# Performance work log

Hardware: AMD Instinct MI355X
Metric: run time of the kernel (lower is better)

The kernel has to match this reference:

```python
import jax, jax.numpy as jnp
import numpy as np

B_SZ, T, N, H = 8, 4096, 256, 512  # batch, seq, num_neurons, d_hidden
RMAX, RMIN = 0.99, 0.4


def _glorot_half(k, shape):
    # VarianceScaling(scale=0.5, mode='fan_avg', distribution='uniform')
    fan_avg = (shape[0] + shape[1]) / 2.0
    limit = float(np.sqrt(3.0 * 0.5 / fan_avg))
    return jax.random.uniform(k, shape, jnp.float32, -limit, limit)


def setup_inputs() -> dict:
    key = jax.random.key(0)
    ks = jax.random.split(key, 8)
    x = jax.random.normal(ks[0], (B_SZ, T, N), jnp.float32)
    C_re = _glorot_half(ks[1], (H, N))
    C_im = _glorot_half(ks[2], (H, N))
    B_re = _glorot_half(ks[3], (N, H))
    B_im = _glorot_half(ks[4], (N, H))
    D = jax.random.normal(ks[5], (N,), jnp.float32)
    numin = float(np.log(-np.log(RMAX)))
    numax = float(np.log(-np.log(RMIN)))
    nu = jax.random.uniform(ks[6], (H,), jnp.float32, numin, numax)
    theta = jax.random.uniform(ks[7], (H,), jnp.float32, 0.0, 3.14 / 10)
    lam_abs = jnp.exp(-jnp.exp(nu))  # |lambda| = |exp(-exp(nu) + i*theta)|
    gamma_log = jnp.log(jnp.sqrt(1.0 - lam_abs ** 2))
    return dict(x=x, B_re=B_re, B_im=B_im, C_re=C_re, C_im=C_im,
                D=D, nu=nu, theta=theta, gamma_log=gamma_log)


def _binary_op(qi, qj):
    A_i, b_i = qi
    A_j, b_j = qj
    return (A_j * A_i, A_j * b_i + b_j)


def reference(x, B_re, B_im, C_re, C_im, D, nu, theta, gamma_log):
    u = x  # adapter is identity since n_in == num_neurons
    lam_log = jax.lax.complex(-jnp.exp(nu), theta)            # (H,) log-lambda
    lam = jnp.exp(lam_log)                                     # (H,) diagonal transition
    gamma = jnp.exp(gamma_log).astype(jnp.complex64)           # (H,)
    Bm = jax.lax.complex(B_re, B_im)                           # (N,H)
    Cm = jax.lax.complex(C_re, C_im)                           # (H,N)
    u_c = u.astype(jnp.complex64)
    bu = gamma * (u_c @ Bm)                                    # (B,T,H) complex64
    A = jnp.broadcast_to(lam, (1, u.shape[1], lam.shape[0]))   # (1,T,H), broadcasts in op
    _, xs = jax.lax.associative_scan(_binary_op, (A, bu), axis=1)  # (B,T,H)
    y = jnp.real(xs @ Cm) + D * u                              # (B,T,N) float32
    return y
```

## Files before the change

kernel.cpp:

```cpp
#include <hip/hip_runtime.h>

#define B_SZ 8
#define T_LEN 4096
#define N_DIM 256
#define H_DIM 512
#define NC 32
#define CL 128
#define ROWS (B_SZ * T_LEN)

#define BM 128
#define BN 128
#define BKg 32

typedef __attribute__((ext_vector_type(4))) float f32x4;
typedef __attribute__((ext_vector_type(8))) short bf16x8;

static __device__ __forceinline__ unsigned short f2bf(float f) {
    unsigned int u = __float_as_uint(f);
    unsigned int r = (u + 0x7FFFu + ((u >> 16) & 1u)) >> 16;
    return (unsigned short)r;
}
static __device__ __forceinline__ float bf2f(unsigned short s) {
    return __uint_as_float(((unsigned int)s) << 16);
}

static __device__ __forceinline__ void lam_of(const float* __restrict__ nu,
                                              const float* __restrict__ theta,
                                              int h, float& lre, float& lim) {
    float r = __expf(-__expf(nu[h]));
    float th = theta[h];
    lre = r * __cosf(th);
    lim = r * __sinf(th);
}

__global__ __launch_bounds__(256) void conv_x(const float4* __restrict__ x, ushort4* __restrict__ xb) {
    int id = blockIdx.x * 256 + threadIdx.x;
    float4 v = x[id];
    ushort4 o;
    o.x = f2bf(v.x); o.y = f2bf(v.y); o.z = f2bf(v.z); o.w = f2bf(v.w);
    xb[id] = o;
}

__global__ __launch_bounds__(256) void conv_Bt(const float* __restrict__ Bre,
                                               const float* __restrict__ Bim,
                                               unsigned short* __restrict__ BT1) {
    int id = blockIdx.x * 256 + threadIdx.x;
    int k = id >> 9, h = id & 511;
    BT1[(long)(2 * h) * 256 + k]     = f2bf(Bre[id]);
    BT1[(long)(2 * h + 1) * 256 + k] = f2bf(Bim[id]);
}

__global__ __launch_bounds__(256) void conv_Ct(const float* __restrict__ Cre,
                                               const float* __restrict__ Cim,
                                               unsigned short* __restrict__ CT) {
    int id = blockIdx.x * 256 + threadIdx.x;
    int h = id >> 8, nn = id & 255;
    CT[(long)nn * 1024 + 2 * h]     = f2bf(Cre[id]);
    CT[(long)nn * 1024 + 2 * h + 1] = f2bf(-Cim[id]);
}

template <int MODE>
__global__ __launch_bounds__(256) void gemm_mfma(const unsigned short* __restrict__ A,
                                                 const unsigned short* __restrict__ Bt,
                                                 int M, int N, int K,
                                                 const float* __restrict__ e0,
                                                 const float* __restrict__ e1,
                                                 const unsigned short* __restrict__ e1b,
                                                 void* __restrict__ out) {
    __shared__ unsigned short As[3][BM * BKg];
    __shared__ unsigned short Bs[3][BN * BKg];
    const int tid = threadIdx.x;
    const int lane = tid & 63;
    const int wave = tid >> 6;
    const int wr = wave >> 1, wc = wave & 1;

    const int nwg = (int)gridDim.x;
    const int cpx = nwg >> 3;
    const int bid = (int)blockIdx.x;
    const int tile = (bid & 7) * cpx + (bid >> 3);

    const int nTilesN = N / BN;
    const long tileM = (long)(tile / nTilesN) * BM;
    const long tileN = (long)(tile % nTilesN) * BN;

    const int rsub = lane >> 2;
    const int sg = 8 * ((lane & 3) ^ ((lane >> 3) & 3));
    const unsigned short* Abase = A + tileM * (long)K + sg;
    const unsigned short* Bbase = Bt + tileN * (long)K + sg;

    auto stage = [&](int buf, int k0) {
#pragma unroll
        for (int cc = 0; cc < 2; ++cc) {
            const int c = wave + cc * 4;
            const int row = c * 16 + rsub;
            const unsigned short* ga = Abase + (long)row * K + k0;
            __builtin_amdgcn_global_load_lds((const __attribute__((address_space(1))) unsigned int*)ga,
                                             (__attribute__((address_space(3))) unsigned int*)(As[buf] + c * 512),
                                             16, 0, 0);
            const unsigned short* gb = Bbase + (long)row * K + k0;
            __builtin_amdgcn_global_load_lds((const __attribute__((address_space(1))) unsigned int*)gb,
                                             (__attribute__((address_space(3))) unsigned int*)(Bs[buf] + c * 512),
                                             16, 0, 0);
        }
    };

    const int rdA = 16 * ((lane >> 4) ^ ((lane >> 1) & 3));

    f32x4 acc[4][4] = {};
    const int nt = K / BKg;

    stage(0, 0);
    stage(1, BKg);

    int cur = 0, pf = 2;
    for (int t = 0; t < nt; ++t) {
        if (t + 2 < nt) {
            stage(pf, (t + 2) * BKg);
            asm volatile("s_waitcnt vmcnt(8)" ::: "memory");
        } else if (t + 1 < nt) {
            asm volatile("s_waitcnt vmcnt(4)" ::: "memory");
        } else {
            asm volatile("s_waitcnt vmcnt(0)" ::: "memory");
        }
        __builtin_amdgcn_s_barrier();
        asm volatile("" ::: "memory");

        bf16x8 af[4], bfr[4];
#pragma unroll
        for (int m = 0; m < 4; ++m) {
            const int row = wr * 64 + m * 16 + (lane & 15);
            af[m] = *(const bf16x8*)((const char*)As[cur] + row * 64 + rdA);
        }
#pragma unroll
        for (int n = 0; n < 4; ++n) {
            const int row = wc * 64 + n * 16 + (lane & 15);
            bfr[n] = *(const bf16x8*)((const char*)Bs[cur] + row * 64 + rdA);
        }
#pragma unroll
        for (int m = 0; m < 4; ++m)
#pragma unroll
            for (int n = 0; n < 4; ++n)
                acc[m][n] = __builtin_amdgcn_mfma_f32_16x16x32_bf16(af[m], bfr[n], acc[m][n], 0, 0, 0);

        asm volatile("" ::: "memory");
        __builtin_amdgcn_s_barrier();
        asm volatile("" ::: "memory");

        cur = (cur == 2) ? 0 : cur + 1;
        pf = (pf == 2) ? 0 : pf + 1;
    }

    if constexpr (MODE == 0) {
        unsigned short* o = (unsigned short*)out;
#pragma unroll
        for (int n = 0; n < 4; ++n) {
            const int gcol = (int)tileN + wc * 64 + n * 16 + (lane & 15);
            const float g = __expf(e0[gcol >> 1]);
#pragma unroll
            for (int m = 0; m < 4; ++m) {
                const long grow0 = tileM + wr * 64 + m * 16 + ((lane >> 4) << 2);
#pragma unroll
                for (int r = 0; r < 4; ++r)
                    o[(grow0 + r) * N + gcol] = f2bf(acc[m][n][r] * g);
            }
        }
    } else {
        float* o = (float*)out;
#pragma unroll
        for (int n = 0; n < 4; ++n) {
            const int gcol = (int)tileN + wc * 64 + n * 16 + (lane & 15);
            const float dv = e0[gcol];
#pragma unroll
            for (int m = 0; m < 4; ++m) {
                const long grow0 = tileM + wr * 64 + m * 16 + ((lane >> 4) << 2);
#pragma unroll
                for (int r = 0; r < 4; ++r) {
                    const long idx = (grow0 + r) * N + gcol;
                    const float uv = e1b ? bf2f(e1b[idx]) : e1[idx];
                    o[idx] = acc[m][n][r] + dv * uv;
                }
            }
        }
    }
}


__global__ __launch_bounds__(256) void k2s_sums(const ushort4* __restrict__ xs4,
                                                float4* __restrict__ sums,
                                                const float* __restrict__ nu,
                                                const float* __restrict__ theta) {
    const int gid = blockIdx.x * 256 + threadIdx.x;
    const int hp = gid & 255;
    const int c = (gid >> 8) & (NC - 1);
    const int b = gid >> 13;
    float lre0, lim0, lre1, lim1;
    lam_of(nu, theta, 2 * hp, lre0, lim0);
    lam_of(nu, theta, 2 * hp + 1, lre1, lim1);
    long base = ((long)b * T_LEN + (long)c * CL) * 256 + hp;
    float a0r = 0.f, a0i = 0.f, a1r = 0.f, a1i = 0.f;
#pragma unroll 4
    for (int i = 0; i < CL; ++i) {
        ushort4 v = xs4[base + (long)i * 256];
        float u0r = bf2f(v.x), u0i = bf2f(v.y), u1r = bf2f(v.z), u1i = bf2f(v.w);
        float n0r = fmaf(lre0, a0r, fmaf(-lim0, a0i, u0r));
        float n0i = fmaf(lre0, a0i, fmaf(lim0, a0r, u0i));
        float n1r = fmaf(lre1, a1r, fmaf(-lim1, a1i, u1r));
        float n1i = fmaf(lre1, a1i, fmaf(lim1, a1r, u1i));
        a0r = n0r; a0i = n0i; a1r = n1r; a1i = n1i;
    }
    sums[((long)b * NC + c) * 256 + hp] = make_float4(a0r, a0i, a1r, a1i);
}

__global__ __launch_bounds__(256) void k2b_carry(const float4* __restrict__ sums,
                                                 float4* __restrict__ carry,
                                                 const float* __restrict__ nu,
                                                 const float* __restrict__ theta) {
    const int gid = blockIdx.x * 256 + threadIdx.x;
    const int hp = gid & 255;
    const int b = gid >> 8;
    float lre0, lim0, lre1, lim1;
    lam_of(nu, theta, 2 * hp, lre0, lim0);
    lam_of(nu, theta, 2 * hp + 1, lre1, lim1);
    float p0r = lre0, p0i = lim0, p1r = lre1, p1i = lim1;
#pragma unroll
    for (int i = 0; i < 7; ++i) {
        float t0 = p0r * p0r - p0i * p0i; p0i = 2.f * p0r * p0i; p0r = t0;
        float t1 = p1r * p1r - p1i * p1i; p1i = 2.f * p1r * p1i; p1r = t1;
    }
    float c0r = 0.f, c0i = 0.f, c1r = 0.f, c1i = 0.f;
    for (int c = 0; c < NC; ++c) {
        long idx = ((long)b * NC + c) * 256 + hp;
        carry[idx] = make_float4(c0r, c0i, c1r, c1i);
        float4 s = sums[idx];
        float t0 = fmaf(p0r, c0r, fmaf(-p0i, c0i, s.x));
        c0i = fmaf(p0r, c0i, fmaf(p0i, c0r, s.y));
        c0r = t0;
        float t1 = fmaf(p1r, c1r, fmaf(-p1i, c1i, s.z));
        c1i = fmaf(p1r, c1i, fmaf(p1i, c1r, s.w));
        c1r = t1;
    }
}

__global__ __launch_bounds__(256) void k2ac_scan(ushort4* __restrict__ xs4,
                                                 const float4* __restrict__ carry,
                                                 const float* __restrict__ nu,
                                                 const float* __restrict__ theta) {
    const int gid = blockIdx.x * 256 + threadIdx.x;
    const int hp = gid & 255;
    const int c = (gid >> 8) & (NC - 1);
    const int b = gid >> 13;
    float lre0, lim0, lre1, lim1;
    lam_of(nu, theta, 2 * hp, lre0, lim0);
    lam_of(nu, theta, 2 * hp + 1, lre1, lim1);
    float4 cr = carry[((long)b * NC + c) * 256 + hp];
    float a0r = cr.x, a0i = cr.y, a1r = cr.z, a1i = cr.w;
    long base = ((long)b * T_LEN + (long)c * CL) * 256 + hp;
#pragma unroll 4
    for (int i = 0; i < CL; ++i) {
        ushort4 v = xs4[base + (long)i * 256];
        float u0r = bf2f(v.x), u0i = bf2f(v.y), u1r = bf2f(v.z), u1i = bf2f(v.w);
        float n0r = fmaf(lre0, a0r, fmaf(-lim0, a0i, u0r));
        float n0i = fmaf(lre0, a0i, fmaf(lim0, a0r, u0i));
        float n1r = fmaf(lre1, a1r, fmaf(-lim1, a1i, u1r));
        float n1i = fmaf(lre1, a1i, fmaf(lim1, a1r, u1i));
        a0r = n0r; a0i = n0i; a1r = n1r; a1i = n1i;
        ushort4 o;
        o.x = f2bf(a0r); o.y = f2bf(a0i); o.z = f2bf(a1r); o.w = f2bf(a1i);
        xs4[base + (long)i * 256] = o;
    }
}

extern "C" void kernel_launch(void* const* d_in, const int* in_sizes, int n_in,
                              void* d_out, int out_size, void* d_ws, size_t ws_size,
                              hipStream_t stream) {
    const float* x         = (const float*)d_in[0];
    const float* Bre       = (const float*)d_in[1];
    const float* Bim       = (const float*)d_in[2];
    const float* Cre       = (const float*)d_in[3];
    const float* Cim       = (const float*)d_in[4];
    const float* Dv        = (const float*)d_in[5];
    const float* nu        = (const float*)d_in[6];
    const float* theta     = (const float*)d_in[7];
    const float* gamma_log = (const float*)d_in[8];
    float* y = (float*)d_out;

    const size_t XS_BYTES  = (size_t)ROWS * H_DIM * 4;
    const size_t REG_BYTES = 2u * 1024 * 1024;
    const size_t XB_BYTES  = (size_t)ROWS * N_DIM * 2;
    unsigned short* xs_us = (unsigned short*)d_ws;
    ushort4* xs4   = (ushort4*)d_ws;
    char* regionA  = (char*)d_ws + XS_BYTES;
    char* regionB  = regionA + REG_BYTES;
    unsigned short* BT1 = (unsigned short*)regionA;
    float4*  sums  = (float4*)regionA;
    unsigned short* CT  = (unsigned short*)regionA;
    float4*  carry = (float4*)regionB;

    const bool xb_in_ws = ws_size >= XS_BYTES + 2 * REG_BYTES + XB_BYTES;
    unsigned short* xb = xb_in_ws ? (unsigned short*)(regionB + REG_BYTES)
                                  : (unsigned short*)d_out;

    conv_x<<<ROWS * N_DIM / 4 / 256, 256, 0, stream>>>((const float4*)x, (ushort4*)xb);
    conv_Bt<<<(N_DIM * H_DIM) / 256, 256, 0, stream>>>(Bre, Bim, BT1);

    gemm_mfma<0><<<(ROWS / BM) * (1024 / BN), 256, 0, stream>>>(xb, BT1, ROWS, 1024, 256,
                                                                gamma_log, nullptr, nullptr, xs_us);
    k2s_sums<<<(B_SZ * NC * 256) / 256, 256, 0, stream>>>(xs4, sums, nu, theta);
    k2b_carry<<<(B_SZ * 256) / 256, 256, 0, stream>>>(sums, carry, nu, theta);
    k2ac_scan<<<(B_SZ * NC * 256) / 256, 256, 0, stream>>>(xs4, carry, nu, theta);

    conv_Ct<<<(H_DIM * N_DIM) / 256, 256, 0, stream>>>(Cre, Cim, CT);

    gemm_mfma<1><<<(ROWS / BM) * (256 / BN), 256, 0, stream>>>(xs_us, CT, ROWS, 256, 1024,
                                                               Dv, x, xb_in_ws ? xb : nullptr, y);
}
```

Baseline: 130.4 us.

## Enlarge GEMM tiles to 256-wide with 8 waves and single-barrier pipeline

```diff
diff --git a/kernel.cpp b/kernel.cpp
--- a/kernel.cpp
+++ b/kernel.cpp
@@ -8,8 +8,6 @@
 #define CL 128
 #define ROWS (B_SZ * T_LEN)
 
-#define BM 128
-#define BN 128
 #define BKg 32
 
 typedef __attribute__((ext_vector_type(4))) float f32x4;
@@ -59,29 +57,37 @@
     CT[(long)nn * 1024 + 2 * h + 1] = f2bf(-Cim[id]);
 }
 
-template <int MODE>
-__global__ __launch_bounds__(256) void gemm_mfma(const unsigned short* __restrict__ A,
-                                                 const unsigned short* __restrict__ Bt,
-                                                 int M, int N, int K,
-                                                 const float* __restrict__ e0,
-                                                 const float* __restrict__ e1,
-                                                 const unsigned short* __restrict__ e1b,
-                                                 void* __restrict__ out) {
-    __shared__ unsigned short As[3][BM * BKg];
-    __shared__ unsigned short Bs[3][BN * BKg];
+template <int MODE, int BMt, int BNt>
+__global__ __launch_bounds__(512, 2) void gemm_mfma(const unsigned short* __restrict__ A,
+                                                    const unsigned short* __restrict__ Bt,
+                                                    int M, int N, int K,
+                                                    const float* __restrict__ e0,
+                                                    const float* __restrict__ e1,
+                                                    const unsigned short* __restrict__ e1b,
+                                                    void* __restrict__ out) {
+    constexpr int WARPS_N = (BNt == 256) ? 4 : 2;
+    constexpr int WARPS_M = 8 / WARPS_N;
+    constexpr int MR = BMt / (WARPS_M * 16);
+    constexpr int NR = BNt / (WARPS_N * 16);
+    constexpr int GA = BMt / 128;
+    constexpr int GB = BNt / 128;
+    constexpr int S = GA + GB;
+
+    __shared__ unsigned short As[3][BMt * BKg];
+    __shared__ unsigned short Bs[3][BNt * BKg];
     const int tid = threadIdx.x;
     const int lane = tid & 63;
     const int wave = tid >> 6;
-    const int wr = wave >> 1, wc = wave & 1;
+    const int wr = wave / WARPS_N, wc = wave % WARPS_N;
 
     const int nwg = (int)gridDim.x;
     const int cpx = nwg >> 3;
     const int bid = (int)blockIdx.x;
     const int tile = (bid & 7) * cpx + (bid >> 3);
 
-    const int nTilesN = N / BN;
-    const long tileM = (long)(tile / nTilesN) * BM;
-    const long tileN = (long)(tile % nTilesN) * BN;
+    const int nTilesN = N / BNt;
+    const long tileM = (long)(tile / nTilesN) * BMt;
+    const long tileN = (long)(tile % nTilesN) * BNt;
 
     const int rsub = lane >> 2;
     const int sg = 8 * ((lane & 3) ^ ((lane >> 3) & 3));
@@ -90,13 +96,18 @@
 
     auto stage = [&](int buf, int k0) {
 #pragma unroll
-        for (int cc = 0; cc < 2; ++cc) {
-            const int c = wave + cc * 4;
+        for (int cc = 0; cc < GA; ++cc) {
+            const int c = wave * GA + cc;
             const int row = c * 16 + rsub;
             const unsigned short* ga = Abase + (long)row * K + k0;
             __builtin_amdgcn_global_load_lds((const __attribute__((address_space(1))) unsigned int*)ga,
                                              (__attribute__((address_space(3))) unsigned int*)(As[buf] + c * 512),
                                              16, 0, 0);
+        }
+#pragma unroll
+        for (int cc = 0; cc < GB; ++cc) {
+            const int c = wave * GB + cc;
+            const int row = c * 16 + rsub;
             const unsigned short* gb = Bbase + (long)row * K + k0;
             __builtin_amdgcn_global_load_lds((const __attribute__((address_space(1))) unsigned int*)gb,
                                              (__attribute__((address_space(3))) unsigned int*)(Bs[buf] + c * 512),
@@ -106,7 +117,7 @@
 
     const int rdA = 16 * ((lane >> 4) ^ ((lane >> 1) & 3));
 
-    f32x4 acc[4][4] = {};
+    f32x4 acc[MR][NR] = {};
     const int nt = K / BKg;
 
     stage(0, 0);
@@ -114,38 +125,35 @@
 
     int cur = 0, pf = 2;
     for (int t = 0; t < nt; ++t) {
-        if (t + 2 < nt) {
-            stage(pf, (t + 2) * BKg);
-            asm volatile("s_waitcnt vmcnt(8)" ::: "memory");
-        } else if (t + 1 < nt) {
-            asm volatile("s_waitcnt vmcnt(4)" ::: "memory");
+        if (t + 1 < nt) {
+            if constexpr (S == 4) asm volatile("s_waitcnt vmcnt(4)" ::: "memory");
+            else                  asm volatile("s_waitcnt vmcnt(3)" ::: "memory");
         } else {
             asm volatile("s_waitcnt vmcnt(0)" ::: "memory");
         }
         __builtin_amdgcn_s_barrier();
         asm volatile("" ::: "memory");
 
-        bf16x8 af[4], bfr[4];
-#pragma unroll
-        for (int m = 0; m < 4; ++m) {
-            const int row = wr * 64 + m * 16 + (lane & 15);
+        if (t + 2 < nt) stage(pf, (t + 2) * BKg);
+
+        bf16x8 af[MR], bfr[NR];
+#pragma unroll
+        for (int m = 0; m < MR; ++m) {
+            const int row = wr * (MR * 16) + m * 16 + (lane & 15);
             af[m] = *(const bf16x8*)((const char*)As[cur] + row * 64 + rdA);
         }
 #pragma unroll
-        for (int n = 0; n < 4; ++n) {
-            const int row = wc * 64 + n * 16 + (lane & 15);
+        for (int n = 0; n < NR; ++n) {
+            const int row = wc * (NR * 16) + n * 16 + (lane & 15);
             bfr[n] = *(const bf16x8*)((const char*)Bs[cur] + row * 64 + rdA);
         }
 #pragma unroll
-        for (int m = 0; m < 4; ++m)
-#pragma unroll
-            for (int n = 0; n < 4; ++n)
+        for (int m = 0; m < MR; ++m)
+#pragma unroll
+            for (int n = 0; n < NR; ++n)
                 acc[m][n] = __builtin_amdgcn_mfma_f32_16x16x32_bf16(af[m], bfr[n], acc[m][n], 0, 0, 0);
 
         asm volatile("" ::: "memory");
-        __builtin_amdgcn_s_barrier();
-        asm volatile("" ::: "memory");
-
         cur = (cur == 2) ? 0 : cur + 1;
         pf = (pf == 2) ? 0 : pf + 1;
     }
@@ -153,12 +161,12 @@
     if constexpr (MODE == 0) {
         unsigned short* o = (unsigned short*)out;
 #pragma unroll
-        for (int n = 0; n < 4; ++n) {
-            const int gcol = (int)tileN + wc * 64 + n * 16 + (lane & 15);
+        for (int n = 0; n < NR; ++n) {
+            const int gcol = (int)tileN + wc * (NR * 16) + n * 16 + (lane & 15);
             const float g = __expf(e0[gcol >> 1]);
 #pragma unroll
-            for (int m = 0; m < 4; ++m) {
-                const long grow0 = tileM + wr * 64 + m * 16 + ((lane >> 4) << 2);
+            for (int m = 0; m < MR; ++m) {
+                const long grow0 = tileM + wr * (MR * 16) + m * 16 + ((lane >> 4) << 2);
 #pragma unroll
                 for (int r = 0; r < 4; ++r)
                     o[(grow0 + r) * N + gcol] = f2bf(acc[m][n][r] * g);
@@ -167,12 +175,12 @@
     } else {
         float* o = (float*)out;
 #pragma unroll
-        for (int n = 0; n < 4; ++n) {
-            const int gcol = (int)tileN + wc * 64 + n * 16 + (lane & 15);
+        for (int n = 0; n < NR; ++n) {
+            const int gcol = (int)tileN + wc * (NR * 16) + n * 16 + (lane & 15);
             const float dv = e0[gcol];
 #pragma unroll
-            for (int m = 0; m < 4; ++m) {
-                const long grow0 = tileM + wr * 64 + m * 16 + ((lane >> 4) << 2);
+            for (int m = 0; m < MR; ++m) {
+                const long grow0 = tileM + wr * (MR * 16) + m * 16 + ((lane >> 4) << 2);
 #pragma unroll
                 for (int r = 0; r < 4; ++r) {
                     const long idx = (grow0 + r) * N + gcol;
@@ -303,14 +311,14 @@
     conv_x<<<ROWS * N_DIM / 4 / 256, 256, 0, stream>>>((const float4*)x, (ushort4*)xb);
     conv_Bt<<<(N_DIM * H_DIM) / 256, 256, 0, stream>>>(Bre, Bim, BT1);
 
-    gemm_mfma<0><<<(ROWS / BM) * (1024 / BN), 256, 0, stream>>>(xb, BT1, ROWS, 1024, 256,
-                                                                gamma_log, nullptr, nullptr, xs_us);
+    gemm_mfma<0, 256, 256><<<(ROWS / 256) * (1024 / 256), 512, 0, stream>>>(
+        xb, BT1, ROWS, 1024, 256, gamma_log, nullptr, nullptr, xs_us);
     k2s_sums<<<(B_SZ * NC * 256) / 256, 256, 0, stream>>>(xs4, sums, nu, theta);
     k2b_carry<<<(B_SZ * 256) / 256, 256, 0, stream>>>(sums, carry, nu, theta);
     k2ac_scan<<<(B_SZ * NC * 256) / 256, 256, 0, stream>>>(xs4, carry, nu, theta);
 
     conv_Ct<<<(H_DIM * N_DIM) / 256, 256, 0, stream>>>(Cre, Cim, CT);
 
-    gemm_mfma<1><<<(ROWS / BM) * (256 / BN), 256, 0, stream>>>(xs_us, CT, ROWS, 256, 1024,
-                                                               Dv, x, xb_in_ws ? xb : nullptr, y);
-}
+    gemm_mfma<1, 256, 128><<<(ROWS / 256) * (256 / 128), 512, 0, stream>>>(
+        xs_us, CT, ROWS, 256, 1024, Dv, x, xb_in_ws ? xb : nullptr, y);
+}
```

Result: slower. 145.8 us (+11.8%).
